# Performance work log

Measured on AMD Instinct MI355X. Metric: run time of the kernel, lower is better.

The kernel has to match this reference:

```python
import jax, jax.numpy as jnp
import numpy as np

EPS = 1e-5

def _rmsnorm(x):
    # BitLinear applies a (non-learnable) RMSNorm to activations before quantization
    return x * jax.lax.rsqrt(jnp.mean(x * x, axis=-1, keepdims=True) + EPS)

def _activation_quant(x):
    # per-token absmax int8 quantization, dequantized back to float
    scale = 127.0 / jnp.clip(jnp.max(jnp.abs(x), axis=-1, keepdims=True), EPS, None)
    return jnp.clip(jnp.round(x * scale), -128, 127) / scale

def _weight_quant(w):
    # absmean ternary {-1,0,1} quantization, dequantized back to float
    scale = 1.0 / jnp.clip(jnp.mean(jnp.abs(w)), EPS, None)
    return jnp.clip(jnp.round(w * scale), -1, 1) / scale

def _bitlinear(x, w):
    xn = _rmsnorm(x)
    # straight-through estimators (identity grads through quantizers)
    xq = xn + jax.lax.stop_gradient(_activation_quant(xn) - xn)
    wq = w + jax.lax.stop_gradient(_weight_quant(w) - w)
    return jnp.einsum('bsd,hd->bsh', xq, wq)

def setup_inputs() -> dict:
    key = jax.random.key(0)
    k1, k2, k3, k4 = jax.random.split(key, 4)
    B, S, D, H = 4, 2048, 4096, 11008
    return {
        'x': jax.random.normal(k1, (B, S, D), dtype=jnp.float32),
        'w_gate': jax.random.normal(k2, (H, D), dtype=jnp.float32) * 0.02,
        'w_up': jax.random.normal(k3, (H, D), dtype=jnp.float32) * 0.02,
        'w_down': jax.random.normal(k4, (D, H), dtype=jnp.float32) * 0.02,
    }

def reference(x, w_gate, w_up, w_down):
    h = jax.nn.silu(_bitlinear(x, w_gate)) * _bitlinear(x, w_up)
    return _bitlinear(h, w_down)
```

## Files before the change

kernel.cpp:

```cpp
#include <hip/hip_runtime.h>
#include <hip/hip_bf16.h>
#include <cstdint>

#define EPS 1e-5

typedef __attribute__((ext_vector_type(4))) int int32x4;

__device__ __forceinline__ void gload(const char* g, char* l) {
  __builtin_amdgcn_global_load_lds(
      (const __attribute__((address_space(1))) unsigned int*)g,
      (__attribute__((address_space(3))) unsigned int*)l, 16, 0, 0);
}

__device__ inline float np_leaf_abs(const float* __restrict__ a, int n) {
  float r[8];
  #pragma unroll
  for (int j = 0; j < 8; j++) r[j] = fabsf(a[j]);
  for (int i = 8; i < n; i += 8) {
    #pragma unroll
    for (int j = 0; j < 8; j++) r[j] += fabsf(a[i + j]);
  }
  return ((r[0] + r[1]) + (r[2] + r[3])) + ((r[4] + r[5]) + (r[6] + r[7]));
}

__global__ __launch_bounds__(256) void np_blocksums(
    const float* __restrict__ w, float* __restrict__ bs) {
  int b = blockIdx.x * 256 + threadIdx.x;
  const float* a = w + (long)b * 344;
  float s0 = np_leaf_abs(a, 80);
  float s1 = np_leaf_abs(a + 80, 88);
  float s2 = np_leaf_abs(a + 168, 88);
  float s3 = np_leaf_abs(a + 256, 88);
  bs[b] = (s0 + s1) + (s2 + s3);
}

__global__ __launch_bounds__(256) void np_tree_partial(
    const float* __restrict__ bs, float* __restrict__ part) {
  __shared__ float sh[256];
  int t = threadIdx.x;
  const float* a = bs + (long)blockIdx.x * 512;
  sh[t] = a[2 * t] + a[2 * t + 1];
  __syncthreads();
  for (int n = 128; n >= 1; n >>= 1) {
    float x = 0.f;
    if (t < n) x = sh[2 * t] + sh[2 * t + 1];
    __syncthreads();
    if (t < n) sh[t] = x;
    __syncthreads();
  }
  if (t == 0) part[blockIdx.x] = sh[0];
}

__global__ __launch_bounds__(128) void np_tree_final(
    const float* __restrict__ part, float* __restrict__ out) {
  __shared__ float sh[128];
  int t = threadIdx.x;
  sh[t] = part[2 * t] + part[2 * t + 1];
  __syncthreads();
  for (int n = 64; n >= 1; n >>= 1) {
    float x = 0.f;
    if (t < n) x = sh[2 * t] + sh[2 * t + 1];
    __syncthreads();
    if (t < n) sh[t] = x;
    __syncthreads();
  }
  if (t == 0) out[0] = sh[0] / 45088768.0f;
}

__global__ __launch_bounds__(256) void quant_w(
    const float* __restrict__ w, const float* __restrict__ mean_ptr,
    char* __restrict__ q, long n4) {
  float scale = 1.0f / fmaxf(*mean_ptr, 1e-5f);
  long i = (long)blockIdx.x * blockDim.x + threadIdx.x;
  long stride = (long)gridDim.x * blockDim.x;
  const float4* w4 = (const float4*)w;
  char4* q4 = (char4*)q;
  for (; i < n4; i += stride) {
    float4 v = w4[i];
    char4 c;
    c.x = (char)(int)fminf(1.f, fmaxf(-1.f, rintf(v.x * scale)));
    c.y = (char)(int)fminf(1.f, fmaxf(-1.f, rintf(v.y * scale)));
    c.z = (char)(int)fminf(1.f, fmaxf(-1.f, rintf(v.z * scale)));
    c.w = (char)(int)fminf(1.f, fmaxf(-1.f, rintf(v.w * scale)));
    q4[i] = c;
  }
}

#define CORR_MAX 1024
#define WIN 1e-6f

__global__ __launch_bounds__(256) void quant_w_down(
    const float* __restrict__ w, const float* __restrict__ mean_ptr,
    char* __restrict__ q, int* __restrict__ cnt,
    int* __restrict__ ck, float* __restrict__ cv) {
  float scale = 1.0f / fmaxf(*mean_ptr, 1e-5f);
  long i0 = ((long)blockIdx.x * blockDim.x + threadIdx.x) * 4;
  long stride = (long)gridDim.x * blockDim.x * 4;
  for (long i = i0; i < 4096L * 11008L; i += stride) {
    char4 c;
    #pragma unroll
    for (int j = 0; j < 4; j++) {
      float t = w[i + j] * scale;
      float qv = fminf(1.f, fmaxf(-1.f, rintf(t)));
      if (fabsf(fabsf(t) - 0.5f) < WIN) {
        qv = 0.f;
        int idx = atomicAdd(cnt, 1);
        if (idx < CORR_MAX) {
          ck[idx] = (int)(i + j);
          cv[idx] = t > 0.f ? 0.5f : -0.5f;
        }
      }
      ((char*)&c)[j] = (char)(int)qv;
    }
    *(char4*)(q + i) = c;
  }
}

__global__ void zero_cnt(int* cnt) { *cnt = 0; }

__global__ __launch_bounds__(64) void apply_corr(
    const int* __restrict__ cnt, const int* __restrict__ ck,
    const float* __restrict__ cv, const char* __restrict__ qh,
    const float* __restrict__ fh, const float* __restrict__ meanw,
    float* __restrict__ out) {
  int r = blockIdx.x * 64 + threadIdx.x;
  float fwd = fmaxf(meanw[2], 1e-5f);
  int n = *cnt; if (n > CORR_MAX) n = CORR_MAX;
  float fr = fh[r] * fwd;
  for (int i = 0; i < n; i++) {
    int flat = ck[i];
    int nn = flat / 11008, kk = flat % 11008;
    float qv = (float)qh[(long)r * 11008 + kk];
    out[(long)r * 4096 + nn] += cv[i] * qv * fr;
  }
}

__device__ inline void block_reduce_sum_max_d(double& s, float& m) {
  #pragma unroll
  for (int off = 1; off < 64; off <<= 1) {
    s += __shfl_xor(s, off, 64);
    m = fmaxf(m, __shfl_xor(m, off, 64));
  }
  __shared__ double ssh[4];
  __shared__ float msh[4];
  int wv = threadIdx.x >> 6;
  if ((threadIdx.x & 63) == 0) { ssh[wv] = s; msh[wv] = m; }
  __syncthreads();
  s = (ssh[0] + ssh[1]) + (ssh[2] + ssh[3]);
  m = fmaxf(fmaxf(msh[0], msh[1]), fmaxf(msh[2], msh[3]));
}

__device__ inline char quant1d(float x, double rn, double s) {
  double t = (double)x * rn;
  double q = rint(t * s);
  q = fmin(127.0, fmax(-128.0, q));
  return (char)(int)q;
}

__global__ __launch_bounds__(256) void act_quant_x(
    const float* __restrict__ x, char* __restrict__ qx, float* __restrict__ fx) {
  const int row = blockIdx.x;
  const float4* xr = (const float4*)(x + (long)row * 4096);
  float4 v[4];
  double ss = 0.0;
  float am = 0.f;
  #pragma unroll
  for (int i = 0; i < 4; i++) {
    v[i] = xr[i * 256 + threadIdx.x];
    ss += ((double)v[i].x * v[i].x + (double)v[i].y * v[i].y) +
          ((double)v[i].z * v[i].z + (double)v[i].w * v[i].w);
    am = fmaxf(am, fmaxf(fmaxf(fabsf(v[i].x), fabsf(v[i].y)),
                         fmaxf(fabsf(v[i].z), fabsf(v[i].w))));
  }
  block_reduce_sum_max_d(ss, am);
  double rn = 1.0 / sqrt(ss / 4096.0 + EPS);
  double den = fmax((double)am * rn, EPS);
  double s = 127.0 / den;
  if (threadIdx.x == 0) fx[row] = (float)(den / 127.0);
  char4* qr = (char4*)(qx + (long)row * 4096);
  #pragma unroll
  for (int i = 0; i < 4; i++) {
    char4 c;
    c.x = quant1d(v[i].x, rn, s);
    c.y = quant1d(v[i].y, rn, s);
    c.z = quant1d(v[i].z, rn, s);
    c.w = quant1d(v[i].w, rn, s);
    qr[i * 256 + threadIdx.x] = c;
  }
}

__global__ __launch_bounds__(256) void act_quant_h(
    const float* __restrict__ h, char* __restrict__ qh, float* __restrict__ fh) {
  const long row = blockIdx.x;
  const float4* hr = (const float4*)(h + row * 11008);
  double ss = 0.0;
  float am = 0.f;
  for (int i = threadIdx.x; i < 2752; i += 256) {
    float4 v = hr[i];
    ss += ((double)v.x * v.x + (double)v.y * v.y) +
          ((double)v.z * v.z + (double)v.w * v.w);
    am = fmaxf(am, fmaxf(fmaxf(fabsf(v.x), fabsf(v.y)),
                         fmaxf(fabsf(v.z), fabsf(v.w))));
  }
  block_reduce_sum_max_d(ss, am);
  double rn = 1.0 / sqrt(ss / 11008.0 + EPS);
  double den = fmax((double)am * rn, EPS);
  double s = 127.0 / den;
  if (threadIdx.x == 0) fh[row] = (float)(den / 127.0);
  char4* qr = (char4*)(qh + row * 11008);
  for (int i = threadIdx.x; i < 2752; i += 256) {
    float4 v = hr[i];
    char4 c;
    c.x = quant1d(v.x, rn, s);
    c.y = quant1d(v.y, rn, s);
    c.z = quant1d(v.z, rn, s);
    c.w = quant1d(v.w, rn, s);
    qr[i] = c;
  }
}


__global__ __launch_bounds__(256, 2) void gemm_gateup(
    const char* __restrict__ qx, const char* __restrict__ qwg, const char* __restrict__ qwu,
    const float* __restrict__ meanw, const float* __restrict__ fx, float* __restrict__ h) {
  __shared__ __align__(16) char As[3][8192];
  __shared__ __align__(16) char Bgs[3][8192];
  __shared__ __align__(16) char Bus[3][8192];
  const int t = threadIdx.x;
  const int lane = t & 63;
  const int wv = t >> 6;
  const int bid = blockIdx.x;
  const int swz = (bid & 7) * 688 + (bid >> 3);
  const int m0 = (swz & 63) * 128;
  const int n0 = (swz >> 6) * 128;
  const int wm = (wv >> 1) * 64;
  const int wn = (wv & 1) * 64;

  const int rowin = lane >> 2;
  const int gcol = (((lane & 3) - ((lane >> 3) & 3)) & 3) * 16;
  const int slot = ((((lane >> 4) + ((lane >> 1) & 3)) & 3) << 4);
  const int lrow = (lane & 15) * 64;

  const char* gA = qx  + (long)(m0 + wv * 32 + rowin) * 4096 + gcol;
  const char* gG = qwg + (long)(n0 + wv * 32 + rowin) * 4096 + gcol;
  const char* gU = qwu + (long)(n0 + wv * 32 + rowin) * 4096 + gcol;
  const long R16 = 16L * 4096;

  int32x4 accg[4][4] = {};
  int32x4 accu[4][4] = {};

  #define STAGE_GU(pb, k0)                                 \
    do {                                                   \
      gload(gA + (k0),       &As [pb][wv * 2048]);         \
      gload(gA + (k0) + R16, &As [pb][wv * 2048 + 1024]);  \
      gload(gG + (k0),       &Bgs[pb][wv * 2048]);         \
      gload(gG + (k0) + R16, &Bgs[pb][wv * 2048 + 1024]);  \
      gload(gU + (k0),       &Bus[pb][wv * 2048]);         \
      gload(gU + (k0) + R16, &Bus[pb][wv * 2048 + 1024]);  \
    } while (0)

  STAGE_GU(0, 0);
  STAGE_GU(1, 64);
  asm volatile("s_waitcnt vmcnt(6)" ::: "memory");
  __builtin_amdgcn_s_barrier();

  for (int ks = 0; ks < 64; ++ks) {
    const int pb = ks % 3;
    const char* ab = &As [pb][0] + wm * 64 + lrow + slot;
    const char* gb = &Bgs[pb][0] + wn * 64 + lrow + slot;
    const char* ub = &Bus[pb][0] + wn * 64 + lrow + slot;
    int32x4 a[4], bg[4], bu[4];
    #pragma unroll
    for (int m = 0; m < 4; m++) a[m] = *(const int32x4*)(ab + m * 1024);
    #pragma unroll
    for (int n = 0; n < 4; n++) bg[n] = *(const int32x4*)(gb + n * 1024);
    #pragma unroll
    for (int n = 0; n < 4; n++) bu[n] = *(const int32x4*)(ub + n * 1024);
    if (ks + 2 < 64) STAGE_GU((ks + 2) % 3, (ks + 2) * 64);
    __builtin_amdgcn_s_setprio(1);
    #pragma unroll
    for (int n = 0; n < 4; n++) {
      #pragma unroll
      for (int m = 0; m < 4; m++) {
        accg[m][n] = __builtin_amdgcn_mfma_i32_16x16x64_i8(a[m], bg[n], accg[m][n], 0, 0, 0);
        accu[m][n] = __builtin_amdgcn_mfma_i32_16x16x64_i8(a[m], bu[n], accu[m][n], 0, 0, 0);
      }
    }
    __builtin_amdgcn_s_setprio(0);
    if (ks < 62)      asm volatile("s_waitcnt vmcnt(6)" ::: "memory");
    else if (ks < 63) asm volatile("s_waitcnt vmcnt(0)" ::: "memory");
    if (ks < 63) __builtin_amdgcn_s_barrier();
  }
  #undef STAGE_GU

  float fwg = fmaxf(meanw[0], 1e-5f);
  float fwu = fmaxf(meanw[1], 1e-5f);
  const int rgrp = lane >> 4;
  const int cidx = lane & 15;
  #pragma unroll
  for (int m = 0; m < 4; m++) {
    #pragma unroll
    for (int r = 0; r < 4; r++) {
      int grow = m0 + wm + m * 16 + rgrp * 4 + r;
      float fxr = fx[grow];
      float sg = fxr * fwg, su = fxr * fwu;
      #pragma unroll
      for (int n = 0; n < 4; n++) {
        float g = (float)accg[m][n][r] * sg;
        float u = (float)accu[m][n][r] * su;
        float hv = g / (1.f + expf(-g)) * u;
        h[(long)grow * 11008 + (n0 + wn + n * 16 + cidx)] = hv;
      }
    }
  }
}

__global__ __launch_bounds__(256, 3) void gemm_down(
    const char* __restrict__ qh, const char* __restrict__ qwd,
    const float* __restrict__ mean_wd, const float* __restrict__ fh,
    float* __restrict__ out) {
  __shared__ __align__(16) char As[3][8192];
  __shared__ __align__(16) char Bs[3][8192];
  const int t = threadIdx.x;
  const int lane = t & 63;
  const int wv = t >> 6;
  const int bid = blockIdx.x;
  const int swz = (bid & 7) * 256 + (bid >> 3);
  const int m0 = (swz & 63) * 128;
  const int n0 = (swz >> 6) * 128;
  const int wm = (wv >> 1) * 64;
  const int wn = (wv & 1) * 64;

  const int rowin = lane >> 2;
  const int gcol = (((lane & 3) - ((lane >> 3) & 3)) & 3) * 16;
  const int slot = ((((lane >> 4) + ((lane >> 1) & 3)) & 3) << 4);
  const int lrow = (lane & 15) * 64;

  const char* gA = qh  + (long)(m0 + wv * 32 + rowin) * 11008 + gcol;
  const char* gB = qwd + (long)(n0 + wv * 32 + rowin) * 11008 + gcol;
  const long R16 = 16L * 11008;

  int32x4 acc[4][4] = {};

  #define STAGE_DN(pb, k0)                                \
    do {                                                  \
      gload(gA + (k0),       &As[pb][wv * 2048]);         \
      gload(gA + (k0) + R16, &As[pb][wv * 2048 + 1024]);  \
      gload(gB + (k0),       &Bs[pb][wv * 2048]);         \
      gload(gB + (k0) + R16, &Bs[pb][wv * 2048 + 1024]);  \
    } while (0)

  STAGE_DN(0, 0);
  STAGE_DN(1, 64);
  asm volatile("s_waitcnt vmcnt(4)" ::: "memory");
  __builtin_amdgcn_s_barrier();

  for (int ks = 0; ks < 172; ++ks) {
    const int pb = ks % 3;
    const char* ab = &As[pb][0] + wm * 64 + lrow + slot;
    const char* bb = &Bs[pb][0] + wn * 64 + lrow + slot;
    int32x4 a[4], b[4];
    #pragma unroll
    for (int m = 0; m < 4; m++) a[m] = *(const int32x4*)(ab + m * 1024);
    #pragma unroll
    for (int n = 0; n < 4; n++) b[n] = *(const int32x4*)(bb + n * 1024);
    if (ks + 2 < 172) STAGE_DN((ks + 2) % 3, (ks + 2) * 64);
    __builtin_amdgcn_s_setprio(1);
    #pragma unroll
    for (int n = 0; n < 4; n++) {
      #pragma unroll
      for (int m = 0; m < 4; m++)
        acc[m][n] = __builtin_amdgcn_mfma_i32_16x16x64_i8(a[m], b[n], acc[m][n], 0, 0, 0);
    }
    __builtin_amdgcn_s_setprio(0);
    if (ks < 170)      asm volatile("s_waitcnt vmcnt(4)" ::: "memory");
    else if (ks < 171) asm volatile("s_waitcnt vmcnt(0)" ::: "memory");
    if (ks < 171) __builtin_amdgcn_s_barrier();
  }
  #undef STAGE_DN

  float fwd = fmaxf(mean_wd[0], 1e-5f);
  const int rgrp = lane >> 4;
  const int cidx = lane & 15;
  #pragma unroll
  for (int m = 0; m < 4; m++) {
    #pragma unroll
    for (int r = 0; r < 4; r++) {
      int grow = m0 + wm + m * 16 + rgrp * 4 + r;
      float f = fh[grow] * fwd;
      #pragma unroll
      for (int n = 0; n < 4; n++) {
        out[(long)grow * 4096 + (n0 + wn + n * 16 + cidx)] =
            (float)acc[m][n][r] * f;
      }
    }
  }
}

extern "C" void kernel_launch(void* const* d_in, const int* in_sizes, int n_in,
                              void* d_out, int out_size, void* d_ws, size_t ws_size,
                              hipStream_t stream) {
  const float* x      = (const float*)d_in[0];
  const float* w_gate = (const float*)d_in[1];
  const float* w_up   = (const float*)d_in[2];
  const float* w_down = (const float*)d_in[3];
  float* out = (float*)d_out;

  const long NW = 11008L * 4096L;
  const long NX = 8192L * 4096L;
  const long NH = 8192L * 11008L;

  char* ws  = (char*)d_ws;
  char* qwg = ws;
  char* qwu = qwg + NW;
  char* qwd = qwu + NW;
  char* qx  = qwd + NW;
  char* qh  = qx + NX;
  float* h  = (float*)(qh + NH);
  float* fx = h + NH;
  float* fh = fx + 8192;
  float* meanw = fh + 8192;
  float* bs    = meanw + 4;
  float* tmp   = bs + 131072;
  int*   ccnt  = (int*)(tmp + 65536);
  int*   ck    = ccnt + 4;
  float* cv    = (float*)(ck + CORR_MAX);

  zero_cnt<<<1, 1, 0, stream>>>(ccnt);

  np_blocksums<<<512, 256, 0, stream>>>(w_gate, bs);
  np_tree_partial<<<256, 256, 0, stream>>>(bs, tmp);
  np_tree_final<<<1, 128, 0, stream>>>(tmp, meanw + 0);
  np_blocksums<<<512, 256, 0, stream>>>(w_up, bs);
  np_tree_partial<<<256, 256, 0, stream>>>(bs, tmp);
  np_tree_final<<<1, 128, 0, stream>>>(tmp, meanw + 1);
  np_blocksums<<<512, 256, 0, stream>>>(w_down, bs);
  np_tree_partial<<<256, 256, 0, stream>>>(bs, tmp);
  np_tree_final<<<1, 128, 0, stream>>>(tmp, meanw + 2);

  quant_w<<<4096, 256, 0, stream>>>(w_gate, meanw + 0, qwg, NW / 4);
  quant_w<<<4096, 256, 0, stream>>>(w_up,   meanw + 1, qwu, NW / 4);
  quant_w_down<<<4096, 256, 0, stream>>>(w_down, meanw + 2, qwd, ccnt, ck, cv);

  act_quant_x<<<8192, 256, 0, stream>>>(x, qx, fx);

  gemm_gateup<<<5504, 256, 0, stream>>>(qx, qwg, qwu, meanw, fx, h);

  act_quant_h<<<8192, 256, 0, stream>>>(h, qh, fh);

  gemm_down<<<2048, 256, 0, stream>>>(qh, qwd, meanw + 2, fh, out);

  apply_corr<<<128, 64, 0, stream>>>(ccnt, ck, cv, qh, fh, meanw, out);
}
```

Before: 1.881 ms.

## Switch GEMMs to 32x32x32 int8 MFMA, widen down-proj tile, cache h row in LDS

Both int8 GEMMs move from 16x16x64 to 32x32x32 MFMA instructions, with new LDS read swizzles and pointer rotation of the triple buffers in place of modulo indexing. The down-projection tile grows from 128x128 to 128x256, which halves the grid and raises B-operand staging and LDS use, and occupancy drops to 2 blocks. act_quant_h caches each h row in shared memory so the second pass does not reread global memory. The aim is fewer MFMA issues and fewer LDS reads per FLOP, plus more reuse of A in the down GEMM. The cost is higher register and LDS pressure and fewer resident waves.

```diff
diff --git a/kernel.cpp b/kernel.cpp
--- a/kernel.cpp
+++ b/kernel.cpp
@@ -5,6 +5,7 @@
 #define EPS 1e-5
 
 typedef __attribute__((ext_vector_type(4))) int int32x4;
+typedef __attribute__((ext_vector_type(16))) int int32x16;
 
 __device__ __forceinline__ void gload(const char* g, char* l) {
   __builtin_amdgcn_global_load_lds(
@@ -191,12 +192,14 @@
 
 __global__ __launch_bounds__(256) void act_quant_h(
     const float* __restrict__ h, char* __restrict__ qh, float* __restrict__ fh) {
+  __shared__ float4 hrow4[2752];
   const long row = blockIdx.x;
   const float4* hr = (const float4*)(h + row * 11008);
   double ss = 0.0;
   float am = 0.f;
   for (int i = threadIdx.x; i < 2752; i += 256) {
     float4 v = hr[i];
+    hrow4[i] = v;
     ss += ((double)v.x * v.x + (double)v.y * v.y) +
           ((double)v.z * v.z + (double)v.w * v.w);
     am = fmaxf(am, fmaxf(fmaxf(fabsf(v.x), fabsf(v.y)),
@@ -209,7 +212,7 @@
   if (threadIdx.x == 0) fh[row] = (float)(den / 127.0);
   char4* qr = (char4*)(qh + row * 11008);
   for (int i = threadIdx.x; i < 2752; i += 256) {
-    float4 v = hr[i];
+    float4 v = hrow4[i];
     char4 c;
     c.x = quant1d(v.x, rn, s);
     c.y = quant1d(v.y, rn, s);
@@ -238,160 +241,195 @@
 
   const int rowin = lane >> 2;
   const int gcol = (((lane & 3) - ((lane >> 3) & 3)) & 3) * 16;
-  const int slot = ((((lane >> 4) + ((lane >> 1) & 3)) & 3) << 4);
-  const int lrow = (lane & 15) * 64;
+  const int r31 = lane & 31;
+  const int rb64 = r31 * 64;
+  const int l5 = lane >> 5;
+  const int rot0 = (((l5 + (r31 >> 1)) & 3)) << 4;
+  const int rot1 = (((2 + l5 + (r31 >> 1)) & 3)) << 4;
 
   const char* gA = qx  + (long)(m0 + wv * 32 + rowin) * 4096 + gcol;
   const char* gG = qwg + (long)(n0 + wv * 32 + rowin) * 4096 + gcol;
   const char* gU = qwu + (long)(n0 + wv * 32 + rowin) * 4096 + gcol;
   const long R16 = 16L * 4096;
 
-  int32x4 accg[4][4] = {};
-  int32x4 accu[4][4] = {};
-
-  #define STAGE_GU(pb, k0)                                 \
-    do {                                                   \
-      gload(gA + (k0),       &As [pb][wv * 2048]);         \
-      gload(gA + (k0) + R16, &As [pb][wv * 2048 + 1024]);  \
-      gload(gG + (k0),       &Bgs[pb][wv * 2048]);         \
-      gload(gG + (k0) + R16, &Bgs[pb][wv * 2048 + 1024]);  \
-      gload(gU + (k0),       &Bus[pb][wv * 2048]);         \
-      gload(gU + (k0) + R16, &Bus[pb][wv * 2048 + 1024]);  \
+  int32x16 accg[2][2] = {};
+  int32x16 accu[2][2] = {};
+
+  char* A0 = &As[0][0];  char* A1 = &As[1][0];  char* A2 = &As[2][0];
+  char* G0 = &Bgs[0][0]; char* G1 = &Bgs[1][0]; char* G2 = &Bgs[2][0];
+  char* U0 = &Bus[0][0]; char* U1 = &Bus[1][0]; char* U2 = &Bus[2][0];
+
+  #define STAGE_GU(pa, pg, pu, k0)                 \
+    do {                                           \
+      gload(gA + (k0),       pa + wv * 2048);      \
+      gload(gA + (k0) + R16, pa + wv * 2048 + 1024); \
+      gload(gG + (k0),       pg + wv * 2048);      \
+      gload(gG + (k0) + R16, pg + wv * 2048 + 1024); \
+      gload(gU + (k0),       pu + wv * 2048);      \
+      gload(gU + (k0) + R16, pu + wv * 2048 + 1024); \
     } while (0)
 
-  STAGE_GU(0, 0);
-  STAGE_GU(1, 64);
+  STAGE_GU(A0, G0, U0, 0);
+  STAGE_GU(A1, G1, U1, 64);
   asm volatile("s_waitcnt vmcnt(6)" ::: "memory");
   __builtin_amdgcn_s_barrier();
 
   for (int ks = 0; ks < 64; ++ks) {
-    const int pb = ks % 3;
-    const char* ab = &As [pb][0] + wm * 64 + lrow + slot;
-    const char* gb = &Bgs[pb][0] + wn * 64 + lrow + slot;
-    const char* ub = &Bus[pb][0] + wn * 64 + lrow + slot;
-    int32x4 a[4], bg[4], bu[4];
-    #pragma unroll
-    for (int m = 0; m < 4; m++) a[m] = *(const int32x4*)(ab + m * 1024);
-    #pragma unroll
-    for (int n = 0; n < 4; n++) bg[n] = *(const int32x4*)(gb + n * 1024);
-    #pragma unroll
-    for (int n = 0; n < 4; n++) bu[n] = *(const int32x4*)(ub + n * 1024);
-    if (ks + 2 < 64) STAGE_GU((ks + 2) % 3, (ks + 2) * 64);
+    int32x4 a[2][2], bg[2][2], bu[2][2];
+    #pragma unroll
+    for (int mi = 0; mi < 2; mi++) {
+      a[mi][0] = *(const int32x4*)(A0 + (wm + mi * 32) * 64 + rb64 + rot0);
+      a[mi][1] = *(const int32x4*)(A0 + (wm + mi * 32) * 64 + rb64 + rot1);
+    }
+    #pragma unroll
+    for (int ni = 0; ni < 2; ni++) {
+      bg[ni][0] = *(const int32x4*)(G0 + (wn + ni * 32) * 64 + rb64 + rot0);
+      bg[ni][1] = *(const int32x4*)(G0 + (wn + ni * 32) * 64 + rb64 + rot1);
+      bu[ni][0] = *(const int32x4*)(U0 + (wn + ni * 32) * 64 + rb64 + rot0);
+      bu[ni][1] = *(const int32x4*)(U0 + (wn + ni * 32) * 64 + rb64 + rot1);
+    }
+    if (ks + 2 < 64) STAGE_GU(A2, G2, U2, (ks + 2) * 64);
     __builtin_amdgcn_s_setprio(1);
     #pragma unroll
-    for (int n = 0; n < 4; n++) {
+    for (int kh = 0; kh < 2; kh++) {
       #pragma unroll
-      for (int m = 0; m < 4; m++) {
-        accg[m][n] = __builtin_amdgcn_mfma_i32_16x16x64_i8(a[m], bg[n], accg[m][n], 0, 0, 0);
-        accu[m][n] = __builtin_amdgcn_mfma_i32_16x16x64_i8(a[m], bu[n], accu[m][n], 0, 0, 0);
+      for (int ni = 0; ni < 2; ni++) {
+        #pragma unroll
+        for (int mi = 0; mi < 2; mi++) {
+          accg[mi][ni] = __builtin_amdgcn_mfma_i32_32x32x32_i8(
+              a[mi][kh], bg[ni][kh], accg[mi][ni], 0, 0, 0);
+          accu[mi][ni] = __builtin_amdgcn_mfma_i32_32x32x32_i8(
+              a[mi][kh], bu[ni][kh], accu[mi][ni], 0, 0, 0);
+        }
       }
     }
     __builtin_amdgcn_s_setprio(0);
     if (ks < 62)      asm volatile("s_waitcnt vmcnt(6)" ::: "memory");
     else if (ks < 63) asm volatile("s_waitcnt vmcnt(0)" ::: "memory");
     if (ks < 63) __builtin_amdgcn_s_barrier();
+    char* tA = A0; A0 = A1; A1 = A2; A2 = tA;
+    char* tG = G0; G0 = G1; G1 = G2; G2 = tG;
+    char* tU = U0; U0 = U1; U1 = U2; U2 = tU;
   }
   #undef STAGE_GU
 
   float fwg = fmaxf(meanw[0], 1e-5f);
   float fwu = fmaxf(meanw[1], 1e-5f);
-  const int rgrp = lane >> 4;
-  const int cidx = lane & 15;
-  #pragma unroll
-  for (int m = 0; m < 4; m++) {
-    #pragma unroll
-    for (int r = 0; r < 4; r++) {
-      int grow = m0 + wm + m * 16 + rgrp * 4 + r;
+  const int col = lane & 31;
+  const int rbase = (lane >> 5) * 4;
+  #pragma unroll
+  for (int mi = 0; mi < 2; mi++) {
+    #pragma unroll
+    for (int reg = 0; reg < 16; reg++) {
+      int grow = m0 + wm + mi * 32 + rbase + (reg & 3) + 8 * (reg >> 2);
       float fxr = fx[grow];
       float sg = fxr * fwg, su = fxr * fwu;
       #pragma unroll
-      for (int n = 0; n < 4; n++) {
-        float g = (float)accg[m][n][r] * sg;
-        float u = (float)accu[m][n][r] * su;
+      for (int ni = 0; ni < 2; ni++) {
+        float g = (float)accg[mi][ni][reg] * sg;
+        float u = (float)accu[mi][ni][reg] * su;
         float hv = g / (1.f + expf(-g)) * u;
-        h[(long)grow * 11008 + (n0 + wn + n * 16 + cidx)] = hv;
+        h[(long)grow * 11008 + (n0 + wn + ni * 32 + col)] = hv;
       }
     }
   }
 }
 
-__global__ __launch_bounds__(256, 3) void gemm_down(
+__global__ __launch_bounds__(256, 2) void gemm_down(
     const char* __restrict__ qh, const char* __restrict__ qwd,
     const float* __restrict__ mean_wd, const float* __restrict__ fh,
     float* __restrict__ out) {
   __shared__ __align__(16) char As[3][8192];
-  __shared__ __align__(16) char Bs[3][8192];
+  __shared__ __align__(16) char Bs[3][16384];
   const int t = threadIdx.x;
   const int lane = t & 63;
   const int wv = t >> 6;
   const int bid = blockIdx.x;
-  const int swz = (bid & 7) * 256 + (bid >> 3);
+  const int swz = (bid & 7) * 128 + (bid >> 3);
   const int m0 = (swz & 63) * 128;
-  const int n0 = (swz >> 6) * 128;
+  const int n0 = (swz >> 6) * 256;
   const int wm = (wv >> 1) * 64;
-  const int wn = (wv & 1) * 64;
+  const int wn = (wv & 1) * 128;
 
   const int rowin = lane >> 2;
   const int gcol = (((lane & 3) - ((lane >> 3) & 3)) & 3) * 16;
-  const int slot = ((((lane >> 4) + ((lane >> 1) & 3)) & 3) << 4);
-  const int lrow = (lane & 15) * 64;
+  const int r31 = lane & 31;
+  const int rb64 = r31 * 64;
+  const int l5 = lane >> 5;
+  const int rot0 = (((l5 + (r31 >> 1)) & 3)) << 4;
+  const int rot1 = (((2 + l5 + (r31 >> 1)) & 3)) << 4;
 
   const char* gA = qh  + (long)(m0 + wv * 32 + rowin) * 11008 + gcol;
-  const char* gB = qwd + (long)(n0 + wv * 32 + rowin) * 11008 + gcol;
+  const char* gB = qwd + (long)(n0 + wv * 64 + rowin) * 11008 + gcol;
   const long R16 = 16L * 11008;
 
-  int32x4 acc[4][4] = {};
-
-  #define STAGE_DN(pb, k0)                                \
-    do {                                                  \
-      gload(gA + (k0),       &As[pb][wv * 2048]);         \
-      gload(gA + (k0) + R16, &As[pb][wv * 2048 + 1024]);  \
-      gload(gB + (k0),       &Bs[pb][wv * 2048]);         \
-      gload(gB + (k0) + R16, &Bs[pb][wv * 2048 + 1024]);  \
+  int32x16 acc[2][4] = {};
+
+  char* A0 = &As[0][0]; char* A1 = &As[1][0]; char* A2 = &As[2][0];
+  char* B0 = &Bs[0][0]; char* B1 = &Bs[1][0]; char* B2 = &Bs[2][0];
+
+  #define STAGE_DN(pa, pb, k0)                          \
+    do {                                                \
+      gload(gA + (k0),           pa + wv * 2048);       \
+      gload(gA + (k0) + R16,     pa + wv * 2048 + 1024);\
+      gload(gB + (k0),           pb + wv * 4096);       \
+      gload(gB + (k0) + R16,     pb + wv * 4096 + 1024);\
+      gload(gB + (k0) + 2 * R16, pb + wv * 4096 + 2048);\
+      gload(gB + (k0) + 3 * R16, pb + wv * 4096 + 3072);\
     } while (0)
 
-  STAGE_DN(0, 0);
-  STAGE_DN(1, 64);
-  asm volatile("s_waitcnt vmcnt(4)" ::: "memory");
+  STAGE_DN(A0, B0, 0);
+  STAGE_DN(A1, B1, 64);
+  asm volatile("s_waitcnt vmcnt(6)" ::: "memory");
   __builtin_amdgcn_s_barrier();
 
   for (int ks = 0; ks < 172; ++ks) {
-    const int pb = ks % 3;
-    const char* ab = &As[pb][0] + wm * 64 + lrow + slot;
-    const char* bb = &Bs[pb][0] + wn * 64 + lrow + slot;
-    int32x4 a[4], b[4];
-    #pragma unroll
-    for (int m = 0; m < 4; m++) a[m] = *(const int32x4*)(ab + m * 1024);
-    #pragma unroll
-    for (int n = 0; n < 4; n++) b[n] = *(const int32x4*)(bb + n * 1024);
-    if (ks + 2 < 172) STAGE_DN((ks + 2) % 3, (ks + 2) * 64);
+    int32x4 a[2][2], b[4][2];
+    #pragma unroll
+    for (int mi = 0; mi < 2; mi++) {
+      a[mi][0] = *(const int32x4*)(A0 + (wm + mi * 32) * 64 + rb64 + rot0);
+      a[mi][1] = *(const int32x4*)(A0 + (wm + mi * 32) * 64 + rb64 + rot1);
+    }
+    #pragma unroll
+    for (int ni = 0; ni < 4; ni++) {
+      b[ni][0] = *(const int32x4*)(B0 + (wn + ni * 32) * 64 + rb64 + rot0);
+      b[ni][1] = *(const int32x4*)(B0 + (wn + ni * 32) * 64 + rb64 + rot1);
+    }
+    if (ks + 2 < 172) STAGE_DN(A2, B2, (ks + 2) * 64);
     __builtin_amdgcn_s_setprio(1);
     #pragma unroll
-    for (int n = 0; n < 4; n++) {
+    for (int kh = 0; kh < 2; kh++) {
       #pragma unroll
-      for (int m = 0; m < 4; m++)
-        acc[m][n] = __builtin_amdgcn_mfma_i32_16x16x64_i8(a[m], b[n], acc[m][n], 0, 0, 0);
+      for (int ni = 0; ni < 4; ni++) {
+        #pragma unroll
+        for (int mi = 0; mi < 2; mi++) {
+          acc[mi][ni] = __builtin_amdgcn_mfma_i32_32x32x32_i8(
+              a[mi][kh], b[ni][kh], acc[mi][ni], 0, 0, 0);
+        }
+      }
     }
     __builtin_amdgcn_s_setprio(0);
-    if (ks < 170)      asm volatile("s_waitcnt vmcnt(4)" ::: "memory");
+    if (ks < 170)      asm volatile("s_waitcnt vmcnt(6)" ::: "memory");
     else if (ks < 171) asm volatile("s_waitcnt vmcnt(0)" ::: "memory");
     if (ks < 171) __builtin_amdgcn_s_barrier();
+    char* tA = A0; A0 = A1; A1 = A2; A2 = tA;
+    char* tB = B0; B0 = B1; B1 = B2; B2 = tB;
   }
   #undef STAGE_DN
 
   float fwd = fmaxf(mean_wd[0], 1e-5f);
-  const int rgrp = lane >> 4;
-  const int cidx = lane & 15;
-  #pragma unroll
-  for (int m = 0; m < 4; m++) {
-    #pragma unroll
-    for (int r = 0; r < 4; r++) {
-      int grow = m0 + wm + m * 16 + rgrp * 4 + r;
+  const int col = lane & 31;
+  const int rbase = (lane >> 5) * 4;
+  #pragma unroll
+  for (int mi = 0; mi < 2; mi++) {
+    #pragma unroll
+    for (int reg = 0; reg < 16; reg++) {
+      int grow = m0 + wm + mi * 32 + rbase + (reg & 3) + 8 * (reg >> 2);
       float f = fh[grow] * fwd;
       #pragma unroll
-      for (int n = 0; n < 4; n++) {
-        out[(long)grow * 4096 + (n0 + wn + n * 16 + cidx)] =
-            (float)acc[m][n][r] * f;
+      for (int ni = 0; ni < 4; ni++) {
+        out[(long)grow * 4096 + (n0 + wn + ni * 32 + col)] =
+            (float)acc[mi][ni][reg] * f;
       }
     }
   }
@@ -448,7 +486,7 @@
 
   act_quant_h<<<8192, 256, 0, stream>>>(h, qh, fh);
 
-  gemm_down<<<2048, 256, 0, stream>>>(qh, qwd, meanw + 2, fh, out);
+  gemm_down<<<1024, 256, 0, stream>>>(qh, qwd, meanw + 2, fh, out);
 
   apply_corr<<<128, 64, 0, stream>>>(ccnt, ck, cv, qh, fh, meanw, out);
 }
```

Measured after the change: 1.736 ms. 1.08x faster.
